# Kernel tuning notes

Measured on AMD Instinct MI355X. Metric: run time of the kernel, lower is better.

The kernel has to match this reference:

```python
import jax, jax.numpy as jnp
import numpy as np

B, D, H, W, K = 16, 512, 64, 64, 32


def setup_inputs() -> dict:
    key = jax.random.key(0)
    k1, k2, k3 = jax.random.split(key, 3)
    x = jax.random.normal(k1, (B, D, H, W), dtype=jnp.float32)
    std1 = 1.0 / float(np.sqrt(K * D))
    codewords = jax.random.uniform(k2, (K, D), dtype=jnp.float32, minval=-std1, maxval=std1)
    scale = jax.random.uniform(k3, (K,), dtype=jnp.float32, minval=-1.0, maxval=0.0)
    return {"x": x, "codewords": codewords, "scale": scale}


def reference(x, codewords, scale):
    b, d = x.shape[0], x.shape[1]
    # [b, d, h, w] -> [b, n, d]
    xr = jnp.transpose(x.reshape(b, d, -1), (0, 2, 1))
    # sl[b,n,k] = scale_k^2 * ||x_bn - c_k||^2, expanded to avoid (b,n,k,d) tensor
    x2 = jnp.sum(xr * xr, axis=-1)                      # [b, n]
    c2 = jnp.sum(codewords * codewords, axis=-1)        # [k]
    xc = jnp.einsum('bnd,kd->bnk', xr, codewords)       # [b, n, k]
    sl = (scale * scale)[None, None, :] * (x2[:, :, None] - 2.0 * xc + c2[None, None, :])
    a = jax.nn.softmax(sl, axis=2)                      # softmax over codewords
    # e[b,k,d] = sum_n a[b,n,k] * (x[b,n,d] - c[k,d])
    e = jnp.einsum('bnk,bnd->bkd', a, xr) - jnp.sum(a, axis=1)[:, :, None] * codewords[None]
    return e
```

## Files before the change

### kernel.cpp

```cpp
#include <hip/hip_runtime.h>
#include <hip/hip_fp16.h>

#define BB 16
#define DD 512
#define NN 4096
#define KK 32
#define TNS 32
#define SUBT 4
#define NGRP 32
#define NBLK (BB*NGRP)
#define ROWX 40
#define ROWA 40

#define OFF_XBUF 0
#define OFF_CLDS 40960
#define OFF_AT   73728
#define OFF_X2P  76288
#define OFF_S2   77312
#define OFF_C2   77440
#define OFF_ASUM 77568
#define LDS_TOTAL 77824


typedef unsigned short u16;
typedef __attribute__((ext_vector_type(8))) short short8v;
typedef __attribute__((ext_vector_type(4))) float f32x4;

#define SYNCL() asm volatile("s_waitcnt lgkmcnt(0)\n\ts_barrier" ::: "memory")

__device__ __forceinline__ unsigned f2bf(float f) {
    union { float f; unsigned u; } v; v.f = f;
    unsigned r = v.u + 0x7fff + ((v.u >> 16) & 1);
    return r >> 16;
}

template <typename PART>
__global__ __launch_bounds__(512, 4)
void k1_fused(const float* __restrict__ x, const float* __restrict__ cw,
              const float* __restrict__ scale,
              float* __restrict__ ws_asum, PART* __restrict__ ws_e) {
    extern __shared__ char smem[];
    u16*   xbuf    = (u16*)(smem + OFF_XBUF);
    u16*   c_lds   = (u16*)(smem + OFF_CLDS);
    u16*   a_t     = (u16*)(smem + OFF_AT);
    float* x2_part = (float*)(smem + OFF_X2P);
    float* s2_l    = (float*)(smem + OFF_S2);
    float* c2_l    = (float*)(smem + OFF_C2);
    float* asum_p  = (float*)(smem + OFF_ASUM);

    const int t = threadIdx.x;
    const int l = t & 63, w = t >> 6;
    const int g = l >> 4, li = l & 15;
    const int blk = blockIdx.x;
    const int b = blk >> 5, grp = blk & 31;
    const int n0 = grp * 128;
    const float* xg = x + (size_t)b * DD * NN + n0;

    const int lr = l >> 3;
    const int lc = l & 7;
    const int cp = lc >> 1, lo = lc & 1;
    const float* xrow = xg + (size_t)(w * 64 + lr) * NN + lc * 4;
    const int wswz = ((cp ^ (lr & 3)) << 4) | (lo << 3);

    const int ck = t >> 4, cseg = t & 15;
    float4 cv[8];
    {
        const float* crow = cw + ck * DD + cseg * 32;
#pragma unroll
        for (int j = 0; j < 8; ++j) cv[j] = *(const float4*)(crow + 4 * j);
    }

    float4 vaA[4], vaB[4];
#pragma unroll
    for (int j = 0; j < 4; ++j) vaA[j] = *(const float4*)(xrow + (size_t)(j * 8) * NN);
#pragma unroll
    for (int j = 0; j < 4; ++j) vaB[j] = *(const float4*)(xrow + (size_t)((j + 4) * 8) * NN);

    {
        float c2p = 0.f;
#pragma unroll
        for (int j = 0; j < 8; ++j)
            c2p += cv[j].x * cv[j].x + cv[j].y * cv[j].y
                 + cv[j].z * cv[j].z + cv[j].w * cv[j].w;
#pragma unroll
        for (int j = 0; j < 4; ++j) {
            uint4 pk;
            asm("v_cvt_pk_bf16_f32 %0, %1, %2" : "=v"(pk.x) : "v"(cv[2*j].x),   "v"(cv[2*j].y));
            asm("v_cvt_pk_bf16_f32 %0, %1, %2" : "=v"(pk.y) : "v"(cv[2*j].z),   "v"(cv[2*j].w));
            asm("v_cvt_pk_bf16_f32 %0, %1, %2" : "=v"(pk.z) : "v"(cv[2*j+1].x), "v"(cv[2*j+1].y));
            asm("v_cvt_pk_bf16_f32 %0, %1, %2" : "=v"(pk.w) : "v"(cv[2*j+1].z), "v"(cv[2*j+1].w));
            const int dch = cseg * 4 + j;
            *(uint4*)(smem + OFF_CLDS + ck * 1024 + ((dch ^ (ck & 7)) << 4)) = pk;
        }
        c2p += __shfl_xor(c2p, 1); c2p += __shfl_xor(c2p, 2);
        c2p += __shfl_xor(c2p, 4); c2p += __shfl_xor(c2p, 8);
        if ((l & 15) == 0) c2_l[ck] = c2p;
        if (t < KK) { float sc = scale[t]; s2_l[t] = sc * sc; }
    }

    f32x4 accB[8];
#pragma unroll
    for (int dt = 0; dt < 8; ++dt) accB[dt] = (f32x4){0.f, 0.f, 0.f, 0.f};
    float asum_acc[8] = {0.f, 0.f, 0.f, 0.f, 0.f, 0.f, 0.f, 0.f};

#pragma unroll
    for (int s = 0; s < SUBT; ++s) {
        {
            float p0 = 0, p1 = 0, p2 = 0, p3 = 0;
#pragma unroll
            for (int j = 0; j < 8; ++j) {
                float4 v = (j < 4) ? vaA[j] : vaB[j - 4];
                uint2 pk;
                asm("v_cvt_pk_bf16_f32 %0, %1, %2" : "=v"(pk.x) : "v"(v.x), "v"(v.y));
                asm("v_cvt_pk_bf16_f32 %0, %1, %2" : "=v"(pk.y) : "v"(v.z), "v"(v.w));
                const int r = w * 64 + j * 8 + lr;
                *(uint2*)(smem + OFF_XBUF + r * 80 + wswz) = pk;
                p0 += v.x * v.x; p1 += v.y * v.y;
                p2 += v.z * v.z; p3 += v.w * v.w;
            }
            p0 += __shfl_xor(p0, 8); p0 += __shfl_xor(p0, 16); p0 += __shfl_xor(p0, 32);
            p1 += __shfl_xor(p1, 8); p1 += __shfl_xor(p1, 16); p1 += __shfl_xor(p1, 32);
            p2 += __shfl_xor(p2, 8); p2 += __shfl_xor(p2, 16); p2 += __shfl_xor(p2, 32);
            p3 += __shfl_xor(p3, 8); p3 += __shfl_xor(p3, 16); p3 += __shfl_xor(p3, 32);
            if (lr == 0) {
                float4 p4 = {p0, p1, p2, p3};
                *(float4*)((char*)smem + OFF_X2P + w * 128 + lc * 16) = p4;
            }
        }
        SYNCL();

        if (s < SUBT - 1) {
#pragma unroll
            for (int j = 0; j < 4; ++j)
                vaA[j] = *(const float4*)(xrow + (size_t)(j * 8) * NN + (s + 1) * TNS);
        }

        if (w < 2) {
            __builtin_amdgcn_s_setprio(1);
            f32x4 accA0 = {0.f, 0.f, 0.f, 0.f}, accA1 = {0.f, 0.f, 0.f, 0.f};
            const int nloc = w * 16 + li;
            const int nc = nloc >> 3, nr = nloc & 7;
            for (int ch = 0; ch < 16; ++ch) {
                const int dbase = ch * 32 + g * 8;
                short8v bf;
#pragma unroll
                for (int j = 0; j < 8; ++j) {
                    const int d = dbase + j;
                    bf[j] = (short)xbuf[d * ROWX + ((nc ^ (d & 3)) << 3) + nr];
                }
                const int csw = ((ch * 4 + g) ^ (li & 7)) << 3;
                short8v a0 = *(const short8v*)(c_lds + li * DD + csw);
                short8v a1 = *(const short8v*)(c_lds + (16 + li) * DD + csw);
                accA0 = __builtin_amdgcn_mfma_f32_16x16x32_bf16(a0, bf, accA0, 0, 0, 0);
                accA1 = __builtin_amdgcn_mfma_f32_16x16x32_bf16(a1, bf, accA1, 0, 0, 0);
            }
            float x2v = 0.f;
#pragma unroll
            for (int p = 0; p < 8; ++p) x2v += x2_part[p * 32 + nloc];
            float sl[8];
            float mx = -3.4e38f;
#pragma unroll
            for (int r = 0; r < 4; ++r) {
                float v0 = s2_l[4 * g + r]      * (x2v - 2.f * accA0[r] + c2_l[4 * g + r]);
                float v1 = s2_l[16 + 4 * g + r] * (x2v - 2.f * accA1[r] + c2_l[16 + 4 * g + r]);
                sl[r] = v0; sl[4 + r] = v1;
                mx = fmaxf(mx, fmaxf(v0, v1));
            }
            mx = fmaxf(mx, __shfl_xor(mx, 16));
            mx = fmaxf(mx, __shfl_xor(mx, 32));
            float sum = 0.f;
#pragma unroll
            for (int i = 0; i < 8; ++i) { sl[i] = __expf(sl[i] - mx); sum += sl[i]; }
            sum += __shfl_xor(sum, 16);
            sum += __shfl_xor(sum, 32);
            const float inv = 1.f / sum;
#pragma unroll
            for (int i = 0; i < 8; ++i) {
                float a = sl[i] * inv;
                int k = (i < 4) ? (4 * g + i) : (16 + 4 * g + (i - 4));
                a_t[k * ROWA + nloc] = (u16)f2bf(a);
                float ssum = a;
                ssum += __shfl_xor(ssum, 1); ssum += __shfl_xor(ssum, 2);
                ssum += __shfl_xor(ssum, 4); ssum += __shfl_xor(ssum, 8);
                asum_acc[i] += ssum;
            }
            __builtin_amdgcn_s_setprio(0);
        }

        if (s < SUBT - 1) {
#pragma unroll
            for (int j = 0; j < 4; ++j)
                vaB[j] = *(const float4*)(xrow + (size_t)((j + 4) * 8) * NN + (s + 1) * TNS);
        }
        SYNCL();

        {
            const int kt = w >> 2, dblk = w & 3;
            short8v af = *(const short8v*)(a_t + (kt * 16 + li) * ROWA + g * 8);
#pragma unroll
            for (int dt = 0; dt < 8; ++dt) {
                const int d = dblk * 128 + dt * 16 + li;
                short8v xf = *(const short8v*)(xbuf + d * ROWX + ((g ^ (d & 3)) << 3));
                accB[dt] = __builtin_amdgcn_mfma_f32_16x16x32_bf16(af, xf, accB[dt], 0, 0, 0);
            }
        }
        SYNCL();
    }

    if (w < 2 && li == 0) {
#pragma unroll
        for (int i = 0; i < 8; ++i) {
            int k = (i < 4) ? (4 * g + i) : (16 + 4 * g + (i - 4));
            asum_p[w * KK + k] = asum_acc[i];
        }
    }
    __syncthreads();
    if (t < KK) ws_asum[(size_t)blk * KK + t] = asum_p[t] + asum_p[KK + t];

    {
        const int kt = w >> 2, dblk = w & 3;
        const size_t ebase = (size_t)blk * KK * DD;
#pragma unroll
        for (int dt = 0; dt < 8; ++dt)
#pragma unroll
            for (int r = 0; r < 4; ++r) {
                int k = kt * 16 + 4 * g + r;
                int d = dblk * 128 + dt * 16 + li;
                ws_e[ebase + (size_t)k * DD + d] = (PART)(accB[dt][r]);
            }
    }
}

__global__ void k2_reduce_h(const __half2* __restrict__ ws_e, const float* __restrict__ ws_asum,
                            const float* __restrict__ cw, float* __restrict__ out) {
    int tid = blockIdx.x * blockDim.x + threadIdx.x;
    int d2 = tid & 255;
    int k = (tid >> 8) & (KK - 1);
    int b = tid >> 13;
    const __half2* pe = ws_e + ((size_t)(b * NGRP) * KK + k) * 256 + d2;
    const float* pa = ws_asum + b * NGRP * KK + k;
    float s0 = 0.f, s1 = 0.f, as = 0.f;
#pragma unroll
    for (int tl = 0; tl < NGRP; ++tl) {
        float2 f = __half22float2(pe[(size_t)tl * KK * 256]);
        s0 += f.x; s1 += f.y;
        as += pa[tl * KK];
    }
    int d = d2 * 2;
    float c0 = cw[k * DD + d], c1 = cw[k * DD + d + 1];
    float2 o; o.x = s0 - as * c0; o.y = s1 - as * c1;
    *(float2*)(out + ((size_t)(b * KK + k) * DD + d)) = o;
}

__global__ void k2_reduce_f(const float* __restrict__ ws_e, const float* __restrict__ ws_asum,
                            const float* __restrict__ cw, float* __restrict__ out) {
    int tid = blockIdx.x * blockDim.x + threadIdx.x;
    int d = tid & (DD - 1);
    int k = (tid >> 9) & (KK - 1);
    int b = tid >> 14;
    float s = 0.f, as = 0.f;
#pragma unroll
    for (int tl = 0; tl < NGRP; ++tl) {
        int blk = b * NGRP + tl;
        s += ws_e[((size_t)blk * KK + k) * DD + d];
        as += ws_asum[(size_t)blk * KK + k];
    }
    out[tid] = s - as * cw[k * DD + d];
}

extern "C" void kernel_launch(void* const* d_in, const int* in_sizes, int n_in,
                              void* d_out, int out_size, void* d_ws, size_t ws_size,
                              hipStream_t stream) {
    const float* x = (const float*)d_in[0];
    const float* cw = (const float*)d_in[1];
    const float* scale = (const float*)d_in[2];
    float* out = (float*)d_out;

    char* ws = (char*)d_ws;
    float* ws_asum = (float*)ws;
    char*  e_ptr   = ws + 65536;

    const size_t need_h = 65536 + (size_t)NBLK * KK * DD * sizeof(__half);

    if (ws_size >= need_h) {
        k1_fused<__half><<<NBLK, 512, LDS_TOTAL, stream>>>(x, cw, scale, ws_asum, (__half*)e_ptr);
        k2_reduce_h<<<(BB * KK * 256) / 256, 256, 0, stream>>>((const __half2*)e_ptr, ws_asum, cw, out);
    } else {
        k1_fused<float><<<NBLK, 512, LDS_TOTAL, stream>>>(x, cw, scale, ws_asum, (float*)e_ptr);
        k2_reduce_f<<<(BB * KK * DD) / 256, 256, 0, stream>>>((const float*)e_ptr, ws_asum, cw, out);
    }
}
```

Before: 38.57 us.

## Repack x LDS tile and use ds_read_b64_tr_b16 for transposed MFMA operands

Changes the bf16 x staging buffer in LDS to an unpadded, swizzled 4-row-group layout, which shrinks the LDS footprint. The first GEMM previously gathered its B operand with eight scalar 16-bit LDS reads per fragment. It now loads it with the transpose-read instruction ds_read_b64_tr_b16, batched four chunks at a time before a single waitcnt. The codeword LDS pack also permutes element order within pairs, presumably to match the transposed operand ordering. This cuts LDS instruction count and bank traffic in the hot loop. The risk is correctness if the new swizzle or permutation does not match the transpose-read semantics.

```diff
diff --git a/kernel.cpp b/kernel.cpp
--- a/kernel.cpp
+++ b/kernel.cpp
@@ -9,24 +9,25 @@
 #define SUBT 4
 #define NGRP 32
 #define NBLK (BB*NGRP)
-#define ROWX 40
 #define ROWA 40
 
 #define OFF_XBUF 0
-#define OFF_CLDS 40960
-#define OFF_AT   73728
-#define OFF_X2P  76288
-#define OFF_S2   77312
-#define OFF_C2   77440
-#define OFF_ASUM 77568
-#define LDS_TOTAL 77824
+#define OFF_CLDS 32768
+#define OFF_AT   65536
+#define OFF_X2P  68096
+#define OFF_S2   69120
+#define OFF_C2   69248
+#define OFF_ASUM 69376
+#define LDS_TOTAL 69632
 
 
 typedef unsigned short u16;
+typedef __attribute__((ext_vector_type(4))) short short4v;
 typedef __attribute__((ext_vector_type(8))) short short8v;
 typedef __attribute__((ext_vector_type(4))) float f32x4;
 
 #define SYNCL() asm volatile("s_waitcnt lgkmcnt(0)\n\ts_barrier" ::: "memory")
+#define PACK2(dst, lo, hi) asm("v_cvt_pk_bf16_f32 %0, %1, %2" : "=v"(dst) : "v"(lo), "v"(hi))
 
 __device__ __forceinline__ unsigned f2bf(float f) {
     union { float f; unsigned u; } v; v.f = f;
@@ -40,7 +41,6 @@
               const float* __restrict__ scale,
               float* __restrict__ ws_asum, PART* __restrict__ ws_e) {
     extern __shared__ char smem[];
-    u16*   xbuf    = (u16*)(smem + OFF_XBUF);
     u16*   c_lds   = (u16*)(smem + OFF_CLDS);
     u16*   a_t     = (u16*)(smem + OFF_AT);
     float* x2_part = (float*)(smem + OFF_X2P);
@@ -58,9 +58,7 @@
 
     const int lr = l >> 3;
     const int lc = l & 7;
-    const int cp = lc >> 1, lo = lc & 1;
     const float* xrow = xg + (size_t)(w * 64 + lr) * NN + lc * 4;
-    const int wswz = ((cp ^ (lr & 3)) << 4) | (lo << 3);
 
     const int ck = t >> 4, cseg = t & 15;
     float4 cv[8];
@@ -84,11 +82,15 @@
                  + cv[j].z * cv[j].z + cv[j].w * cv[j].w;
 #pragma unroll
         for (int j = 0; j < 4; ++j) {
+            const float4 cA = cv[2 * j], cB = cv[2 * j + 1];
             uint4 pk;
-            asm("v_cvt_pk_bf16_f32 %0, %1, %2" : "=v"(pk.x) : "v"(cv[2*j].x),   "v"(cv[2*j].y));
-            asm("v_cvt_pk_bf16_f32 %0, %1, %2" : "=v"(pk.y) : "v"(cv[2*j].z),   "v"(cv[2*j].w));
-            asm("v_cvt_pk_bf16_f32 %0, %1, %2" : "=v"(pk.z) : "v"(cv[2*j+1].x), "v"(cv[2*j+1].y));
-            asm("v_cvt_pk_bf16_f32 %0, %1, %2" : "=v"(pk.w) : "v"(cv[2*j+1].z), "v"(cv[2*j+1].w));
+            if ((j & 1) == 0) {
+                PACK2(pk.x, cA.x, cA.y); PACK2(pk.y, cA.z, cA.w);
+                PACK2(pk.z, cB.y, cB.x); PACK2(pk.w, cB.w, cB.z);
+            } else {
+                PACK2(pk.x, cA.z, cA.w); PACK2(pk.y, cA.x, cA.y);
+                PACK2(pk.z, cB.w, cB.z); PACK2(pk.w, cB.y, cB.x);
+            }
             const int dch = cseg * 4 + j;
             *(uint4*)(smem + OFF_CLDS + ck * 1024 + ((dch ^ (ck & 7)) << 4)) = pk;
         }
@@ -111,10 +113,13 @@
             for (int j = 0; j < 8; ++j) {
                 float4 v = (j < 4) ? vaA[j] : vaB[j - 4];
                 uint2 pk;
-                asm("v_cvt_pk_bf16_f32 %0, %1, %2" : "=v"(pk.x) : "v"(v.x), "v"(v.y));
-                asm("v_cvt_pk_bf16_f32 %0, %1, %2" : "=v"(pk.y) : "v"(v.z), "v"(v.w));
+                PACK2(pk.x, v.x, v.y);
+                PACK2(pk.y, v.z, v.w);
                 const int r = w * 64 + j * 8 + lr;
-                *(uint2*)(smem + OFF_XBUF + r * 80 + wswz) = pk;
+                const int D2 = r >> 2;
+                const int slot = (lr & 3) ^ (D2 & 3);
+                *(uint2*)(smem + OFF_XBUF + (D2 * 2 + (lc >> 2)) * 128
+                          + slot * 32 + (lc & 3) * 8) = pk;
                 p0 += v.x * v.x; p1 += v.y * v.y;
                 p2 += v.z * v.z; p3 += v.w * v.w;
             }
@@ -139,20 +144,32 @@
             __builtin_amdgcn_s_setprio(1);
             f32x4 accA0 = {0.f, 0.f, 0.f, 0.f}, accA1 = {0.f, 0.f, 0.f, 0.f};
             const int nloc = w * 16 + li;
-            const int nc = nloc >> 3, nr = nloc & 7;
-            for (int ch = 0; ch < 16; ++ch) {
-                const int dbase = ch * 32 + g * 8;
-                short8v bf;
-#pragma unroll
-                for (int j = 0; j < 8; ++j) {
-                    const int d = dbase + j;
-                    bf[j] = (short)xbuf[d * ROWX + ((nc ^ (d & 3)) << 3) + nr];
+            const unsigned xb0 = (unsigned)(uintptr_t)smem + OFF_XBUF
+                               + g * 512 + w * 128 + li * 2;
+#pragma unroll
+            for (int cg = 0; cg < 4; ++cg) {
+                short4v tA[8];
+#pragma unroll
+                for (int u = 0; u < 4; ++u) {
+                    const unsigned a0a = xb0 + (cg * 4 + u) * 2048;
+                    asm volatile("ds_read_b64_tr_b16 %0, %1"
+                                 : "=v"(tA[2 * u]) : "v"(a0a));
+                    asm volatile("ds_read_b64_tr_b16 %0, %1"
+                                 : "=v"(tA[2 * u + 1]) : "v"(a0a + 256));
                 }
-                const int csw = ((ch * 4 + g) ^ (li & 7)) << 3;
-                short8v a0 = *(const short8v*)(c_lds + li * DD + csw);
-                short8v a1 = *(const short8v*)(c_lds + (16 + li) * DD + csw);
-                accA0 = __builtin_amdgcn_mfma_f32_16x16x32_bf16(a0, bf, accA0, 0, 0, 0);
-                accA1 = __builtin_amdgcn_mfma_f32_16x16x32_bf16(a1, bf, accA1, 0, 0, 0);
+                asm volatile("s_waitcnt lgkmcnt(0)" ::: "memory");
+                __builtin_amdgcn_sched_barrier(0);
+#pragma unroll
+                for (int u = 0; u < 4; ++u) {
+                    const int ch = cg * 4 + u;
+                    short8v bf = __builtin_shufflevector(tA[2 * u], tA[2 * u + 1],
+                                                         0, 1, 2, 3, 4, 5, 6, 7);
+                    const int csw = ((ch * 4 + g) ^ (li & 7)) << 3;
+                    short8v a0 = *(const short8v*)(c_lds + li * DD + csw);
+                    short8v a1 = *(const short8v*)(c_lds + (16 + li) * DD + csw);
+                    accA0 = __builtin_amdgcn_mfma_f32_16x16x32_bf16(a0, bf, accA0, 0, 0, 0);
+                    accA1 = __builtin_amdgcn_mfma_f32_16x16x32_bf16(a1, bf, accA1, 0, 0, 0);
+                }
             }
             float x2v = 0.f;
 #pragma unroll
@@ -197,10 +214,12 @@
         {
             const int kt = w >> 2, dblk = w & 3;
             short8v af = *(const short8v*)(a_t + (kt * 16 + li) * ROWA + g * 8);
+            const int slotB = (li & 3) ^ (li >> 2);
+            const char* xbB = smem + OFF_XBUF + (dblk * 32 + (li >> 2)) * 256
+                            + (g >> 1) * 128 + slotB * 32 + (g & 1) * 16;
 #pragma unroll
             for (int dt = 0; dt < 8; ++dt) {
-                const int d = dblk * 128 + dt * 16 + li;
-                short8v xf = *(const short8v*)(xbuf + d * ROWX + ((g ^ (d & 3)) << 3));
+                short8v xf = *(const short8v*)(xbB + dt * 1024);
                 accB[dt] = __builtin_amdgcn_mfma_f32_16x16x32_bf16(af, xf, accB[dt], 0, 0, 0);
             }
         }
```

Result: slower. 44.55 us (+15.5%).
